# Kernel optimization log

Measured on AMD Instinct MI355X. Metric: run time of the kernel, lower is better.

## Reference

```python
import jax, jax.numpy as jnp
import numpy as np

NUM_HEADS = 4
KEY_DIM = 64
D_MODEL = 256
OUTPUT_DIM = 256


def setup_inputs() -> dict:
    key = jax.random.key(0)
    ks = jax.random.split(key, 11)
    B, T, D = 16, 1024, D_MODEL
    HD = NUM_HEADS * KEY_DIM
    s = 0.02
    return {
        "query": jax.random.normal(ks[0], (B, T, D), jnp.float32),
        "key": jax.random.normal(ks[1], (B, T, D), jnp.float32),
        "value": jax.random.normal(ks[2], (B, T, D), jnp.float32),
        "Wq": jax.random.normal(ks[3], (D, HD), jnp.float32) * s,
        "bq": jnp.zeros((HD,), jnp.float32),
        "Wk": jax.random.normal(ks[4], (D, HD), jnp.float32) * s,
        "bk": jnp.zeros((HD,), jnp.float32),
        "Wv": jax.random.normal(ks[5], (D, KEY_DIM), jnp.float32) * s,
        "bv": jnp.zeros((KEY_DIM,), jnp.float32),
        "Wo": jax.random.normal(ks[6], (HD, OUTPUT_DIM), jnp.float32) * s,
        "bo": jnp.zeros((OUTPUT_DIM,), jnp.float32),
    }


def reference(query, key, value, Wq, bq, Wk, bk, Wv, bv, Wo, bo):
    B, Tq, _ = query.shape
    Tk = key.shape[1]
    H, Dk = NUM_HEADS, KEY_DIM
    # projections
    q = (query @ Wq + bq).reshape(B, Tq, H, Dk)  # [B,Tq,H,Dk]
    k = (key @ Wk + bk).reshape(B, Tk, H, Dk)    # [B,Tk,H,Dk]
    v = value @ Wv + bv                           # [B,Tk,Dk] shared across heads
    scale = jnp.asarray(Dk, q.dtype) ** -0.5
    # scores [B,H,Tq,Tk]
    score = jnp.einsum("bqhd,bkhd->bhqk", q, k) * scale
    attn = jax.nn.softmax(score, axis=-1)
    # broadcast-V attention: [B,H,Tq,Tk] x [B,Tk,Dk] -> [B,H,Tq,Dk]
    out = jnp.einsum("bhqk,bkd->bhqd", attn, v)
    out = out.transpose(0, 2, 1, 3).reshape(B, Tq, H * Dk)
    return out @ Wo + bo
```

## Files before the change

### kernel.cpp

```cpp
#include <hip/hip_runtime.h>
#include <hip/hip_bf16.h>


typedef __attribute__((ext_vector_type(8))) short short8;
typedef __attribute__((ext_vector_type(4))) float f32x4;
typedef __attribute__((ext_vector_type(16))) float f32x16;

__device__ __forceinline__ short f2bf(float x) {
    return __builtin_bit_cast(short, __float2bfloat16(x));
}

__device__ __forceinline__ float exp2_fast(float x) {
#if __has_builtin(__builtin_amdgcn_exp2f)
    return __builtin_amdgcn_exp2f(x);
#else
    float r; asm("v_exp_f32 %0, %1" : "=v"(r) : "v"(x)); return r;
#endif
}

__device__ __forceinline__ f32x4 mfma16(short8 a, short8 b, f32x4 c) {
    return __builtin_amdgcn_mfma_f32_16x16x32_bf16(a, b, c, 0, 0, 0);
}
__device__ __forceinline__ f32x16 mfma32(short8 a, short8 b, f32x16 c) {
    return __builtin_amdgcn_mfma_f32_32x32x16_bf16(a, b, c, 0, 0, 0);
}

__device__ __forceinline__ int cvtpk(float lo, float hi) {
    int r; asm("v_cvt_pk_bf16_f32 %0, %1, %2" : "=v"(r) : "v"(lo), "v"(hi));
    return r;
}
__device__ __forceinline__ void swap32(int& a, int& b) {
    asm("v_permlane32_swap_b32 %0, %1" : "+v"(a), "+v"(b));
}

__device__ __forceinline__ short8 half_frag(const f32x16& s, int base) {
    int d0 = cvtpk(s[base + 0], s[base + 1]);
    int d1 = cvtpk(s[base + 2], s[base + 3]);
    int d2 = cvtpk(s[base + 4], s[base + 5]);
    int d3 = cvtpk(s[base + 6], s[base + 7]);
    swap32(d0, d2);
    swap32(d1, d3);
    int4 v = { d0, d1, d2, d3 };
    return __builtin_bit_cast(short8, v);
}

__device__ __forceinline__ float sum16(const f32x16& e) {
    return (((e[0] + e[1]) + (e[2] + e[3])) + ((e[4] + e[5]) + (e[6] + e[7])))
         + (((e[8] + e[9]) + (e[10] + e[11])) + ((e[12] + e[13]) + (e[14] + e[15])));
}

#define QSCALE 0.18033688011112042f

__global__ void prep_weights(const float* __restrict__ Wq, const float* __restrict__ Wk,
                             const float* __restrict__ Wv, const float* __restrict__ Wo,
                             short* __restrict__ WqtF, short* __restrict__ WktF,
                             short* __restrict__ WvtF, short* __restrict__ WotF) {
    int tid = blockIdx.x * 256 + threadIdx.x;
    int k = tid >> 8, n = tid & 255;
    int off = ((n >> 6) << 14) + (((n >> 4) & 3) << 12) + ((k >> 5) << 9)
            + (((k >> 3) & 3) << 7) + ((n & 15) << 3) + (k & 7);
    WqtF[off] = f2bf(Wq[k * 256 + n] * QSCALE);
    WktF[off] = f2bf(Wk[k * 256 + n]);
    int offo = ((n >> 5) << 13) + ((k >> 4) << 9) + (((k & 15) >> 3) << 8)
             + ((n & 31) << 3) + (k & 7);
    WotF[offo] = f2bf(Wo[k * 256 + n]);
    if (n < 64) {
        int offv = ((n >> 4) << 12) + ((k >> 5) << 9) + (((k >> 3) & 3) << 7)
                 + ((n & 15) << 3) + (k & 7);
        WvtF[offv] = f2bf(Wv[k * 64 + n]);
    }
}

__global__ __launch_bounds__(256) void proj_all(
        const float* __restrict__ query, const float* __restrict__ key_,
        const float* __restrict__ value,
        const short* __restrict__ WqtF, const short* __restrict__ WktF,
        const short* __restrict__ WvtF,
        const float* __restrict__ bq, const float* __restrict__ bk,
        const float* __restrict__ bv,
        short* __restrict__ qf, short* __restrict__ kf, short* __restrict__ vf) {
    __shared__ short At[8192];
    const int tid = threadIdx.x;
    const int lane = tid & 63, wave = tid >> 6;
    const int u = lane >> 4, r16 = lane & 15;
    const int m0 = blockIdx.x * 32;
    const int task = blockIdx.y;

    const float* A = task == 0 ? query : (task == 1 ? key_ : value);

    #pragma unroll
    for (int j = 0; j < 4; ++j) {
        int p8 = j * 8 + ((wave >> 1) << 2) + u;
        int row = ((wave & 1) << 4) + r16;
        const float* src = A + (m0 + row) * 256 + p8 * 8;
        float4 a0 = *(const float4*)src;
        float4 a1 = *(const float4*)(src + 4);
        short8 w;
        w[0] = f2bf(a0.x); w[1] = f2bf(a0.y); w[2] = f2bf(a0.z); w[3] = f2bf(a0.w);
        w[4] = f2bf(a1.x); w[5] = f2bf(a1.y); w[6] = f2bf(a1.z); w[7] = f2bf(a1.w);
        int dst = ((p8 >> 2) << 10) + ((wave & 1) << 9) + ((p8 & 3) << 7) + (r16 << 3);
        *(short8*)&At[dst] = w;
    }

    const int b = m0 >> 10, t32 = (m0 >> 5) & 31;

    if (task < 2) {
        const short* WtF = task == 0 ? WqtF : WktF;
        const float* bias = task == 0 ? bq : bk;
        const float bscale = task == 0 ? QSCALE : 1.0f;
        short* outF = task == 0 ? qf : kf;
        const short* wb = WtF + (wave << 14);

        short8 bf8[4];
        #pragma unroll
        for (int g = 0; g < 4; ++g) bf8[g] = *(const short8*)&wb[(g << 12) + lane * 8];
        __syncthreads();

        f32x4 acc[2][4] = {};
        #pragma unroll
        for (int kk = 0; kk < 8; ++kk) {
            short8 af[2], nb[4];
            #pragma unroll
            for (int f = 0; f < 2; ++f) af[f] = *(const short8*)&At[(kk << 10) + (f << 9) + lane * 8];
            if (kk < 7) {
                #pragma unroll
                for (int g = 0; g < 4; ++g) nb[g] = *(const short8*)&wb[(g << 12) + ((kk + 1) << 9) + lane * 8];
            }
            #pragma unroll
            for (int f = 0; f < 2; ++f)
                #pragma unroll
                for (int g = 0; g < 4; ++g)
                    acc[f][g] = mfma16(af[f], bf8[g], acc[f][g]);
            #pragma unroll
            for (int g = 0; g < 4; ++g) bf8[g] = nb[g];
        }

        float bvv[4];
        #pragma unroll
        for (int g = 0; g < 4; ++g) bvv[g] = bias[(wave << 6) + 16 * g + r16] * bscale;
        short* ob = outF + ((((b << 2) + wave) << 5) + t32) * 2048;
        #pragma unroll
        for (int f = 0; f < 2; ++f)
            #pragma unroll
            for (int g = 0; g < 4; ++g)
                #pragma unroll
                for (int rr = 0; rr < 4; ++rr)
                    ob[(g << 9) + ((r16 >> 3) << 8) + (16 * f + 4 * u + rr) * 8 + (r16 & 7)]
                        = f2bf(acc[f][g][rr] + bvv[g]);
    } else {
        const int fr = wave >> 1;
        short8 bf8[2];
        #pragma unroll
        for (int z = 0; z < 2; ++z) {
            int dg = ((wave & 1) << 1) + z;
            bf8[z] = *(const short8*)&WvtF[(dg << 12) + lane * 8];
        }
        __syncthreads();

        f32x4 acc[2] = {};
        #pragma unroll
        for (int kk = 0; kk < 8; ++kk) {
            short8 af = *(const short8*)&At[(kk << 10) + (fr << 9) + lane * 8];
            short8 nb[2];
            if (kk < 7) {
                #pragma unroll
                for (int z = 0; z < 2; ++z) {
                    int dg = ((wave & 1) << 1) + z;
                    nb[z] = *(const short8*)&WvtF[(dg << 12) + ((kk + 1) << 9) + lane * 8];
                }
            }
            #pragma unroll
            for (int z = 0; z < 2; ++z) acc[z] = mfma16(af, bf8[z], acc[z]);
            bf8[0] = nb[0]; bf8[1] = nb[1];
        }

        short* ob = vf + ((b << 5) + t32) * 2048;
        #pragma unroll
        for (int z = 0; z < 2; ++z) {
            int dg = ((wave & 1) << 1) + z;
            float bvv = bv[16 * dg + r16];
            #pragma unroll
            for (int rr = 0; rr < 4; ++rr) {
                int tl = 4 * u + rr;
                ob[((dg >> 1) << 10) + (fr << 9) + ((tl >> 3) << 8)
                   + ((16 * (dg & 1) + r16) << 3) + (tl & 7)]
                    = f2bf(acc[z][rr] + bvv);
            }
        }
    }
}

__global__ __launch_bounds__(512, 4) void attn_og(const short* __restrict__ qF,
        const short* __restrict__ kF, const short* __restrict__ vF,
        const short* __restrict__ WoF, const float* __restrict__ bo,
        float* __restrict__ outp) {
    __shared__ float4 ocm4s[2048];
    __shared__ float lcm[256];
    __shared__ short At[8192];
    const int tid = threadIdx.x;
    const int lane = tid & 63, wave = tid >> 6;
    const int h = wave & 3, kvh = wave >> 2;
    const int u2 = lane >> 5, n31 = lane & 31;

    const int L = (blockIdx.x & 7) * 64 + (blockIdx.x >> 3);
    const int b = L >> 5, qt = L & 31;

    const short* qb = qF + ((((b << 2) + h) << 5) + qt) * 2048;
    short8 Q[4];
    #pragma unroll
    for (int c = 0; c < 4; ++c) Q[c] = *(const short8*)&qb[(c << 9) + lane * 8];

    const short* kb = kF + ((((b << 2) + h) << 5) + (kvh << 4)) * 2048;
    const short* vb = vF + (((b << 5) + (kvh << 4))) * 2048;

    f32x16 aO0 = {}, aO1 = {};
    float l = 0.f;

    for (int i = 0; i < 16; ++i) {
        const short* kt = kb + i * 2048;
        const short* vt = vb + i * 2048;
        short8 kfr[4], vfr[4];
        #pragma unroll
        for (int c = 0; c < 4; ++c) {
            kfr[c] = *(const short8*)&kt[(c << 9) + lane * 8];
            vfr[c] = *(const short8*)&vt[(c << 9) + lane * 8];
        }

        f32x16 S = {};
        __builtin_amdgcn_s_setprio(1);
        S = mfma32(kfr[0], Q[0], S);
        S = mfma32(kfr[1], Q[1], S);
        S = mfma32(kfr[2], Q[2], S);
        S = mfma32(kfr[3], Q[3], S);
        __builtin_amdgcn_s_setprio(0);

        #pragma unroll
        for (int j = 0; j < 16; ++j) S[j] = exp2_fast(S[j]);
        l += sum16(S);

        short8 p0 = half_frag(S, 0);
        short8 p1 = half_frag(S, 8);

        __builtin_amdgcn_s_setprio(1);
        aO0 = mfma32(vfr[0], p0, aO0);
        aO0 = mfma32(vfr[1], p1, aO0);
        aO1 = mfma32(vfr[2], p0, aO1);
        aO1 = mfma32(vfr[3], p1, aO1);
        __builtin_amdgcn_s_setprio(0);
    }

    l += __shfl_xor(l, 32);

    if (kvh == 1) {
        #pragma unroll
        for (int j4 = 0; j4 < 4; ++j4) {
            float4 w0 = { aO0[4 * j4], aO0[4 * j4 + 1], aO0[4 * j4 + 2], aO0[4 * j4 + 3] };
            float4 w1 = { aO1[4 * j4], aO1[4 * j4 + 1], aO1[4 * j4 + 2], aO1[4 * j4 + 3] };
            ocm4s[(((h << 1) + 0) * 4 + j4) * 64 + lane] = w0;
            ocm4s[(((h << 1) + 1) * 4 + j4) * 64 + lane] = w1;
        }
        lcm[(h << 6) + lane] = l;
    }
    __syncthreads();

    if (kvh == 0) {
        #pragma unroll
        for (int j4 = 0; j4 < 4; ++j4) {
            float4 r0 = ocm4s[(((h << 1) + 0) * 4 + j4) * 64 + lane];
            float4 r1 = ocm4s[(((h << 1) + 1) * 4 + j4) * 64 + lane];
            aO0[4 * j4 + 0] += r0.x; aO0[4 * j4 + 1] += r0.y;
            aO0[4 * j4 + 2] += r0.z; aO0[4 * j4 + 3] += r0.w;
            aO1[4 * j4 + 0] += r1.x; aO1[4 * j4 + 1] += r1.y;
            aO1[4 * j4 + 2] += r1.z; aO1[4 * j4 + 3] += r1.w;
        }
        float li = 1.0f / (l + lcm[(h << 6) + lane]);
        #pragma unroll
        for (int j = 0; j < 16; ++j) { aO0[j] *= li; aO1[j] *= li; }

        short8 a00 = half_frag(aO0, 0), a01 = half_frag(aO0, 8);
        short8 a10 = half_frag(aO1, 0), a11 = half_frag(aO1, 8);
        *(short8*)&At[(((h << 2) + 0) << 9) + lane * 8] = a00;
        *(short8*)&At[(((h << 2) + 1) << 9) + lane * 8] = a01;
        *(short8*)&At[(((h << 2) + 2) << 9) + lane * 8] = a10;
        *(short8*)&At[(((h << 2) + 3) << 9) + lane * 8] = a11;
    }
    __syncthreads();

    const short* wo0 = WoF + wave * 8192;
    f32x16 acc2 = {};
    #pragma unroll
    for (int kc = 0; kc < 16; ++kc) {
        short8 a = *(const short8*)&At[(kc << 9) + lane * 8];
        short8 w0 = *(const short8*)&wo0[(kc << 9) + lane * 8];
        acc2 = mfma32(a, w0, acc2);
    }

    const int m0 = L << 5;
    {
        float bv0 = bo[wave * 32 + n31];
        #pragma unroll
        for (int r = 0; r < 16; ++r) {
            int q = (r & 3) + 8 * (r >> 2) + 4 * u2;
            outp[(m0 + q) * 256 + wave * 32 + n31] = acc2[r] + bv0;
        }
    }
}

extern "C" void kernel_launch(void* const* d_in, const int* in_sizes, int n_in,
                              void* d_out, int out_size, void* d_ws, size_t ws_size,
                              hipStream_t stream) {
    (void)in_sizes; (void)n_in; (void)out_size; (void)ws_size;
    const float* query = (const float*)d_in[0];
    const float* key_  = (const float*)d_in[1];
    const float* value = (const float*)d_in[2];
    const float* Wq = (const float*)d_in[3];
    const float* bq = (const float*)d_in[4];
    const float* Wk = (const float*)d_in[5];
    const float* bk = (const float*)d_in[6];
    const float* Wv = (const float*)d_in[7];
    const float* bv = (const float*)d_in[8];
    const float* Wo = (const float*)d_in[9];
    const float* bo = (const float*)d_in[10];
    float* outp = (float*)d_out;

    short* wsp  = (short*)d_ws;
    short* WqtF = wsp;
    short* WktF = wsp + 65536;
    short* WotF = wsp + 131072;
    short* WvtF = wsp + 196608;
    short* qf   = wsp + 212992;
    short* kf   = wsp + 4407296;
    short* vf   = wsp + 8601600;

    hipLaunchKernelGGL(prep_weights, dim3(256), dim3(256), 0, stream,
                       Wq, Wk, Wv, Wo, WqtF, WktF, WvtF, WotF);
    hipLaunchKernelGGL(proj_all, dim3(512, 3), dim3(256), 0, stream,
                       query, key_, value, WqtF, WktF, WvtF, bq, bk, bv, qf, kf, vf);
    hipLaunchKernelGGL(attn_og, dim3(512), dim3(512), 0, stream,
                       qf, kf, vf, WotF, bo, outp);
}
```

Baseline: 56.66 us.

## Stage K/V tiles through LDS with async triple buffer, two query tiles per block

The attention kernel now has each block handle two query tiles (one per group of 4 waves) instead of splitting the key range across wave groups. The shared K tiles for all 4 heads and the V tile are staged into LDS with global_load_lds into a triple-buffered pipeline, with vmcnt waits and barriers between steps. This removes the cross-wave partial-sum merge through shared memory and halves redundant K/V global loads per query tile. In exchange it uses more LDS, adds a barrier every iteration, halves the grid to 256 blocks, and gives up the key-range parallelism, so fewer waves are available to hide latency.

```diff
diff --git a/kernel.cpp b/kernel.cpp
--- a/kernel.cpp
+++ b/kernel.cpp
@@ -31,6 +31,12 @@
 }
 __device__ __forceinline__ void swap32(int& a, int& b) {
     asm("v_permlane32_swap_b32 %0, %1" : "+v"(a), "+v"(b));
+}
+
+__device__ __forceinline__ void gll16(const float4* gsrc, float4* ldst) {
+    __builtin_amdgcn_global_load_lds(
+        (const __attribute__((address_space(1))) void*)gsrc,
+        (__attribute__((address_space(3))) void*)ldst, 16, 0, 0);
 }
 
 __device__ __forceinline__ short8 half_frag(const f32x16& s, int base) {
@@ -190,49 +196,78 @@
     }
 }
 
-__global__ __launch_bounds__(512, 4) void attn_og(const short* __restrict__ qF,
+__global__ __launch_bounds__(512, 2) void attn_og(const short* __restrict__ qF,
         const short* __restrict__ kF, const short* __restrict__ vF,
         const short* __restrict__ WoF, const float* __restrict__ bo,
         float* __restrict__ outp) {
-    __shared__ float4 ocm4s[2048];
-    __shared__ float lcm[256];
-    __shared__ short At[8192];
+    __shared__ float4 stage[3840];
+    short* At = (short*)stage;
     const int tid = threadIdx.x;
     const int lane = tid & 63, wave = tid >> 6;
-    const int h = wave & 3, kvh = wave >> 2;
+    const int h = wave & 3, qh = wave >> 2;
     const int u2 = lane >> 5, n31 = lane & 31;
 
-    const int L = (blockIdx.x & 7) * 64 + (blockIdx.x >> 3);
-    const int b = L >> 5, qt = L & 31;
-
-    const short* qb = qF + ((((b << 2) + h) << 5) + qt) * 2048;
+    const int L = (blockIdx.x & 7) * 32 + (blockIdx.x >> 3);
+    const int b = L >> 4, qt = L & 15;
+
+    const short* qb = qF + ((((b << 2) + h) << 5) + (qt << 1) + qh) * 2048;
     short8 Q[4];
     #pragma unroll
     for (int c = 0; c < 4; ++c) Q[c] = *(const short8*)&qb[(c << 9) + lane * 8];
 
-    const short* kb = kF + ((((b << 2) + h) << 5) + (kvh << 4)) * 2048;
-    const short* vb = vF + (((b << 5) + (kvh << 4))) * 2048;
+    const float4* kb4 = (const float4*)kF + (b << 2) * 32 * 256;
+    const float4* vb4 = (const float4*)vF + (b << 5) * 256;
+
+    #define STAGE(t, bp)                                                        \
+        {                                                                       \
+            _Pragma("unroll")                                                   \
+            for (int j_ = 0; j_ < 3; ++j_) {                                    \
+                int ch_ = wave + 8 * j_;                                        \
+                if (ch_ < 20) {                                                 \
+                    const float4* src_;                                         \
+                    float4* dst_;                                               \
+                    if (ch_ < 16) {                                             \
+                        src_ = kb4 + ((ch_ >> 2) * 32 + (t)) * 256              \
+                             + ((ch_ & 3) << 6) + lane;                         \
+                        dst_ = (bp) + (ch_ << 6);                               \
+                    } else {                                                    \
+                        src_ = vb4 + (t) * 256 + ((ch_ - 16) << 6) + lane;      \
+                        dst_ = (bp) + 1024 + ((ch_ - 16) << 6);                 \
+                    }                                                           \
+                    gll16(src_, dst_);                                          \
+                }                                                               \
+            }                                                                   \
+        }
+
+    STAGE(0, stage)
+    STAGE(1, stage + 1280)
+    if (wave < 4) asm volatile("s_waitcnt vmcnt(3)" ::: "memory");
+    else          asm volatile("s_waitcnt vmcnt(2)" ::: "memory");
+    __builtin_amdgcn_s_barrier();
 
     f32x16 aO0 = {}, aO1 = {};
     float l = 0.f;
 
-    for (int i = 0; i < 16; ++i) {
-        const short* kt = kb + i * 2048;
-        const short* vt = vb + i * 2048;
-        short8 kfr[4], vfr[4];
-        #pragma unroll
-        for (int c = 0; c < 4; ++c) {
-            kfr[c] = *(const short8*)&kt[(c << 9) + lane * 8];
-            vfr[c] = *(const short8*)&vt[(c << 9) + lane * 8];
-        }
+    for (int t = 0; t < 32; ++t) {
+        const int cur = t % 3;
+        if (t + 2 < 32) {
+            float4* nb = stage + ((t + 2) % 3) * 1280;
+            STAGE(t + 2, nb)
+        }
+
+        const short* Kh = (const short*)(stage + cur * 1280) + (h << 11);
+        const short* Vb = (const short*)(stage + cur * 1280) + 8192;
+
+        short8 kfr[4];
+        #pragma unroll
+        for (int c = 0; c < 4; ++c)
+            kfr[c] = *(const short8*)&Kh[(c << 9) + lane * 8];
 
         f32x16 S = {};
-        __builtin_amdgcn_s_setprio(1);
         S = mfma32(kfr[0], Q[0], S);
         S = mfma32(kfr[1], Q[1], S);
         S = mfma32(kfr[2], Q[2], S);
         S = mfma32(kfr[3], Q[3], S);
-        __builtin_amdgcn_s_setprio(0);
 
         #pragma unroll
         for (int j = 0; j < 16; ++j) S[j] = exp2_fast(S[j]);
@@ -241,67 +276,69 @@
         short8 p0 = half_frag(S, 0);
         short8 p1 = half_frag(S, 8);
 
-        __builtin_amdgcn_s_setprio(1);
+        short8 vfr[4];
+        #pragma unroll
+        for (int c = 0; c < 4; ++c)
+            vfr[c] = *(const short8*)&Vb[(c << 9) + lane * 8];
+
         aO0 = mfma32(vfr[0], p0, aO0);
         aO0 = mfma32(vfr[1], p1, aO0);
         aO1 = mfma32(vfr[2], p0, aO1);
         aO1 = mfma32(vfr[3], p1, aO1);
-        __builtin_amdgcn_s_setprio(0);
-    }
+
+        if (t < 30) {
+            if (wave < 4) asm volatile("s_waitcnt vmcnt(3)" ::: "memory");
+            else          asm volatile("s_waitcnt vmcnt(2)" ::: "memory");
+            __builtin_amdgcn_s_barrier();
+        } else if (t == 30) {
+            asm volatile("s_waitcnt vmcnt(0)" ::: "memory");
+            __builtin_amdgcn_s_barrier();
+        }
+    }
+    #undef STAGE
 
     l += __shfl_xor(l, 32);
-
-    if (kvh == 1) {
-        #pragma unroll
-        for (int j4 = 0; j4 < 4; ++j4) {
-            float4 w0 = { aO0[4 * j4], aO0[4 * j4 + 1], aO0[4 * j4 + 2], aO0[4 * j4 + 3] };
-            float4 w1 = { aO1[4 * j4], aO1[4 * j4 + 1], aO1[4 * j4 + 2], aO1[4 * j4 + 3] };
-            ocm4s[(((h << 1) + 0) * 4 + j4) * 64 + lane] = w0;
-            ocm4s[(((h << 1) + 1) * 4 + j4) * 64 + lane] = w1;
-        }
-        lcm[(h << 6) + lane] = l;
-    }
+    float li = 1.0f / l;
+    #pragma unroll
+    for (int j = 0; j < 16; ++j) { aO0[j] *= li; aO1[j] *= li; }
+
+    short8 a0 = half_frag(aO0, 0), a1 = half_frag(aO0, 8);
+    short8 a2 = half_frag(aO1, 0), a3 = half_frag(aO1, 8);
+
     __syncthreads();
 
-    if (kvh == 0) {
-        #pragma unroll
-        for (int j4 = 0; j4 < 4; ++j4) {
-            float4 r0 = ocm4s[(((h << 1) + 0) * 4 + j4) * 64 + lane];
-            float4 r1 = ocm4s[(((h << 1) + 1) * 4 + j4) * 64 + lane];
-            aO0[4 * j4 + 0] += r0.x; aO0[4 * j4 + 1] += r0.y;
-            aO0[4 * j4 + 2] += r0.z; aO0[4 * j4 + 3] += r0.w;
-            aO1[4 * j4 + 0] += r1.x; aO1[4 * j4 + 1] += r1.y;
-            aO1[4 * j4 + 2] += r1.z; aO1[4 * j4 + 3] += r1.w;
-        }
-        float li = 1.0f / (l + lcm[(h << 6) + lane]);
-        #pragma unroll
-        for (int j = 0; j < 16; ++j) { aO0[j] *= li; aO1[j] *= li; }
-
-        short8 a00 = half_frag(aO0, 0), a01 = half_frag(aO0, 8);
-        short8 a10 = half_frag(aO1, 0), a11 = half_frag(aO1, 8);
-        *(short8*)&At[(((h << 2) + 0) << 9) + lane * 8] = a00;
-        *(short8*)&At[(((h << 2) + 1) << 9) + lane * 8] = a01;
-        *(short8*)&At[(((h << 2) + 2) << 9) + lane * 8] = a10;
-        *(short8*)&At[(((h << 2) + 3) << 9) + lane * 8] = a11;
+    {
+        short* atw = At + (qh << 13) + ((h << 2) << 9) + lane * 8;
+        *(short8*)&atw[0 * 512] = a0;
+        *(short8*)&atw[1 * 512] = a1;
+        *(short8*)&atw[2 * 512] = a2;
+        *(short8*)&atw[3 * 512] = a3;
     }
     __syncthreads();
 
-    const short* wo0 = WoF + wave * 8192;
-    f32x16 acc2 = {};
+    const int qtile = wave >> 2, np = wave & 3;
+    const short* at = At + (qtile << 13);
+    const short* wo0 = WoF + (2 * np) * 8192;
+    const short* wo1 = wo0 + 8192;
+    f32x16 acc20 = {}, acc21 = {};
     #pragma unroll
     for (int kc = 0; kc < 16; ++kc) {
-        short8 a = *(const short8*)&At[(kc << 9) + lane * 8];
+        short8 a = *(const short8*)&at[(kc << 9) + lane * 8];
         short8 w0 = *(const short8*)&wo0[(kc << 9) + lane * 8];
-        acc2 = mfma32(a, w0, acc2);
-    }
-
-    const int m0 = L << 5;
+        short8 w1 = *(const short8*)&wo1[(kc << 9) + lane * 8];
+        acc20 = mfma32(a, w0, acc20);
+        acc21 = mfma32(a, w1, acc21);
+    }
+
+    const int m0 = (L << 6) + (qtile << 5);
     {
-        float bv0 = bo[wave * 32 + n31];
+        float bv0 = bo[(2 * np) * 32 + n31];
+        float bv1 = bo[(2 * np + 1) * 32 + n31];
         #pragma unroll
         for (int r = 0; r < 16; ++r) {
             int q = (r & 3) + 8 * (r >> 2) + 4 * u2;
-            outp[(m0 + q) * 256 + wave * 32 + n31] = acc2[r] + bv0;
+            outp[(m0 + q) * 256 + (2 * np) * 32 + n31] = acc20[r] + bv0;
+            outp[(m0 + q) * 256 + (2 * np + 1) * 32 + n31] = acc21[r] + bv1;
         }
     }
 }
@@ -336,6 +373,6 @@
                        Wq, Wk, Wv, Wo, WqtF, WktF, WvtF, WotF);
     hipLaunchKernelGGL(proj_all, dim3(512, 3), dim3(256), 0, stream,
                        query, key_, value, WqtF, WktF, WvtF, bq, bk, bv, qf, kf, vf);
-    hipLaunchKernelGGL(attn_og, dim3(512), dim3(512), 0, stream,
+    hipLaunchKernelGGL(attn_og, dim3(256), dim3(512), 0, stream,
                        qf, kf, vf, WotF, bo, outp);
 }
```

Measured after the change: 57.37 us. About the same (+1.3%).
